# Performance work log

Measured on AMD Instinct MI355X. Metric: run time of the kernel, lower is better.

Reference implementation:

```python
import jax, jax.numpy as jnp
import numpy as np

B, T, C, H = 8, 2048, 1024, 64

def setup_inputs() -> dict:
    key = jax.random.key(0)
    k1, k2, k3, k4 = jax.random.split(key, 4)
    sc = 1.0 / np.sqrt(C)
    return {
        "x": jax.random.normal(k1, (B, T, C), dtype=jnp.float32),
        "Wk": jax.random.normal(k2, (C, H), dtype=jnp.float32) * sc,
        "Wq": jax.random.normal(k3, (C, H), dtype=jnp.float32) * sc,
        "Wv": jax.random.normal(k4, (C, H), dtype=jnp.float32) * sc,
    }

def reference(x, Wk, Wq, Wv):
    # bias-free projections: [B,T,C] @ [C,H] -> [B,T,H]
    k = jnp.einsum("btc,ch->bth", x, Wk)
    q = jnp.einsum("btc,ch->bth", x, Wq)
    v = jnp.einsum("btc,ch->bth", x, Wv)
    scale = Wk.shape[-1] ** -0.5  # head_size ** -0.5
    # attention scores [B,T,T]
    wei = jnp.einsum("bth,bsh->bts", q, k) * scale
    # causal mask: position t attends to s <= t
    Tn = x.shape[1]
    causal = jnp.tril(jnp.ones((Tn, Tn), dtype=bool))
    wei = jnp.where(causal[None, :, :], wei, jnp.float32(-jnp.inf))
    wei = jax.nn.softmax(wei, axis=-1)
    out = jnp.einsum("bts,bsh->bth", wei, v)  # [B,T,H]
    return out
```

## Files before the change

### kernel.cpp

```cpp
#include <hip/hip_runtime.h>
#include <math.h>

#define Bb 8
#define Tt 2048
#define Cc 1024
#define Hh 64

typedef __attribute__((ext_vector_type(8))) short short8;
typedef __attribute__((ext_vector_type(4))) float f32x4;

static __device__ __forceinline__ unsigned short f2bf(float f) {
    union { float f; unsigned u; } v; v.f = f;
    unsigned r = (v.u + 0x7FFFu + ((v.u >> 16) & 1u)) >> 16;
    return (unsigned short)r;
}

__global__ __launch_bounds__(256)
void wconv_kernel(const float* __restrict__ Wk, const float* __restrict__ Wq,
                  const float* __restrict__ Wv, unsigned short* __restrict__ WbT)
{
    const int n = blockIdx.x;
    const int h = n & 63;
    const float* W; float scale = 1.0f;
    if (n < 64)       { W = Wq; scale = 0.125f; }
    else if (n < 128) { W = Wk; }
    else              { W = Wv; }
    #pragma unroll
    for (int i = 0; i < 4; ++i) {
        const int k = threadIdx.x + (i << 8);
        WbT[n * 1024 + k] = f2bf(W[k * 64 + h] * scale);
    }
}

__global__ __launch_bounds__(512)
void proj_kernel(const float* __restrict__ x, const unsigned short* __restrict__ WbT,
                 unsigned short* __restrict__ qb, unsigned short* __restrict__ kb,
                 unsigned short* __restrict__ vb)
{
    __shared__ unsigned short As[64][72];
    __shared__ unsigned short Bs[192][72];

    const int tid  = threadIdx.x;
    const int row0 = blockIdx.x * 64;
    const int lane = tid & 63;
    const int w    = tid >> 6;
    const int wm   = w >> 2;
    const int wn   = w & 3;
    const int fr   = lane & 15;
    const int fko  = (lane >> 4) << 3;

    f32x4 acc[2][3];
    #pragma unroll
    for (int i = 0; i < 2; ++i)
        #pragma unroll
        for (int j = 0; j < 3; ++j) acc[i][j] = (f32x4){0.f, 0.f, 0.f, 0.f};

    for (int k0 = 0; k0 < Cc; k0 += 64) {
        #pragma unroll
        for (int i = 0; i < 2; ++i) {
            const int c  = tid + (i << 9);
            const int r  = c >> 4;
            const int ko = (c & 15) << 2;
            const float4 xv = *reinterpret_cast<const float4*>(
                &x[(size_t)(row0 + r) * Cc + k0 + ko]);
            ushort4 h4;
            h4.x = f2bf(xv.x); h4.y = f2bf(xv.y); h4.z = f2bf(xv.z); h4.w = f2bf(xv.w);
            *reinterpret_cast<ushort4*>(&As[r][ko]) = h4;
        }
        #pragma unroll
        for (int i = 0; i < 3; ++i) {
            const int c  = tid + (i << 9);
            const int r  = c >> 3;
            const int ko = (c & 7) << 3;
            const short8 bv = *reinterpret_cast<const short8*>(
                &WbT[(size_t)r * 1024 + k0 + ko]);
            *reinterpret_cast<short8*>(&Bs[r][ko]) = bv;
        }
        __syncthreads();

        #pragma unroll
        for (int sub = 0; sub < 2; ++sub) {
            short8 af[2], bf[3];
            #pragma unroll
            for (int mf = 0; mf < 2; ++mf)
                af[mf] = *reinterpret_cast<const short8*>(
                    &As[wm * 32 + mf * 16 + fr][sub * 32 + fko]);
            #pragma unroll
            for (int nf = 0; nf < 3; ++nf)
                bf[nf] = *reinterpret_cast<const short8*>(
                    &Bs[wn * 48 + nf * 16 + fr][sub * 32 + fko]);
            #pragma unroll
            for (int mf = 0; mf < 2; ++mf)
                #pragma unroll
                for (int nf = 0; nf < 3; ++nf)
                    acc[mf][nf] = __builtin_amdgcn_mfma_f32_16x16x32_bf16(
                        af[mf], bf[nf], acc[mf][nf], 0, 0, 0);
        }
        __syncthreads();
    }

    #pragma unroll
    for (int mf = 0; mf < 2; ++mf)
        #pragma unroll
        for (int nf = 0; nf < 3; ++nf) {
            const int col = wn * 48 + nf * 16 + fr;
            const int mat = col >> 6;
            const int h   = col & 63;
            unsigned short* dst = (mat == 0) ? qb : (mat == 1) ? kb : vb;
            #pragma unroll
            for (int r = 0; r < 4; ++r) {
                const int row = row0 + wm * 32 + mf * 16 + ((lane >> 4) << 2) + r;
                dst[(size_t)row * 64 + h] = f2bf(acc[mf][nf][r]);
            }
        }
}

__global__ __launch_bounds__(256)
void vtrans_kernel(const unsigned short* __restrict__ vb,
                   unsigned short* __restrict__ vt)
{
    __shared__ unsigned short ls[64][72];
    const int tid = threadIdx.x;
    const int t0  = blockIdx.x * 64;
    const int b   = blockIdx.y;

    #pragma unroll
    for (int i = 0; i < 2; ++i) {
        const int c  = tid + (i << 8);
        const int r  = c >> 3;
        const int ho = (c & 7) << 3;
        *reinterpret_cast<short8*>(&ls[r][ho]) =
            *reinterpret_cast<const short8*>(&vb[((size_t)b * Tt + t0 + r) * 64 + ho]);
    }
    __syncthreads();
    #pragma unroll
    for (int i = 0; i < 2; ++i) {
        const int c  = tid + (i << 8);
        const int h  = c >> 3;
        const int to = (c & 7) << 3;
        short8 v;
        #pragma unroll
        for (int j = 0; j < 8; ++j) v[j] = (short)ls[to + j][h];
        *reinterpret_cast<short8*>(&vt[((size_t)b * 64 + h) * Tt + t0 + to]) = v;
    }
}

__global__ __launch_bounds__(256)
void attn_kernel(const unsigned short* __restrict__ qb,
                 const unsigned short* __restrict__ kb,
                 const unsigned short* __restrict__ vt,
                 float* __restrict__ out)
{
    __shared__ float smem[9216];

    const int tid  = threadIdx.x;
    const int b    = blockIdx.y;
    const int qt   = 63 - blockIdx.x;
    const int lane = tid & 63;
    const int w    = tid >> 6;
    const int fr   = lane & 15;
    const int fg   = lane >> 4;
    const int fko  = fg << 3;
    const int ktmax = qt >> 1;

    short8 aq[2][2];
    #pragma unroll
    for (int mf = 0; mf < 2; ++mf)
        #pragma unroll
        for (int hs = 0; hs < 2; ++hs) {
            const size_t gq = (size_t)b * Tt + qt * 32 + mf * 16 + fr;
            aq[mf][hs] = *reinterpret_cast<const short8*>(&qb[gq * 64 + hs * 32 + fko]);
        }

    float mrun[2][4], lrun[2][4];
    f32x4 O[2][4];
    #pragma unroll
    for (int mf = 0; mf < 2; ++mf) {
        #pragma unroll
        for (int r = 0; r < 4; ++r) { mrun[mf][r] = -INFINITY; lrun[mf][r] = 0.f; }
        #pragma unroll
        for (int nh = 0; nh < 4; ++nh) O[mf][nh] = (f32x4){0.f, 0.f, 0.f, 0.f};
    }

    unsigned short* Pw = (unsigned short*)smem + w * 2304;

    for (int kt = w; kt <= ktmax; kt += 4) {
        short8 bk[4][2], bv[4][2];
        #pragma unroll
        for (int nf = 0; nf < 4; ++nf)
            #pragma unroll
            for (int hs = 0; hs < 2; ++hs) {
                const size_t gk = (size_t)b * Tt + kt * 64 + nf * 16 + fr;
                bk[nf][hs] = *reinterpret_cast<const short8*>(&kb[gk * 64 + hs * 32 + fko]);
            }
        #pragma unroll
        for (int nh = 0; nh < 4; ++nh)
            #pragma unroll
            for (int ks = 0; ks < 2; ++ks) {
                const size_t gv = ((size_t)b * 64 + nh * 16 + fr) * Tt
                                  + kt * 64 + ks * 32 + fko;
                bv[nh][ks] = *reinterpret_cast<const short8*>(&vt[gv]);
            }

        const f32x4 zero = (f32x4){0.f, 0.f, 0.f, 0.f};
        f32x4 s[2][4];
        #pragma unroll
        for (int mf = 0; mf < 2; ++mf)
            #pragma unroll
            for (int nf = 0; nf < 4; ++nf) {
                f32x4 t = __builtin_amdgcn_mfma_f32_16x16x32_bf16(aq[mf][0], bk[nf][0], zero, 0, 0, 0);
                s[mf][nf] = __builtin_amdgcn_mfma_f32_16x16x32_bf16(aq[mf][1], bk[nf][1], t, 0, 0, 0);
            }

        if (kt == ktmax) {
            #pragma unroll
            for (int mf = 0; mf < 2; ++mf)
                #pragma unroll
                for (int nf = 0; nf < 4; ++nf)
                    #pragma unroll
                    for (int r = 0; r < 4; ++r) {
                        const int key  = kt * 64 + nf * 16 + fr;
                        const int qrow = qt * 32 + mf * 16 + (fg << 2) + r;
                        if (key > qrow) s[mf][nf][r] = -INFINITY;
                    }
        }

        float alpha[2][4];
        #pragma unroll
        for (int mf = 0; mf < 2; ++mf)
            #pragma unroll
            for (int r = 0; r < 4; ++r) {
                float tmax = fmaxf(fmaxf(s[mf][0][r], s[mf][1][r]),
                                   fmaxf(s[mf][2][r], s[mf][3][r]));
                #pragma unroll
                for (int off = 1; off < 16; off <<= 1)
                    tmax = fmaxf(tmax, __shfl_xor(tmax, off, 64));
                const float mn = fmaxf(mrun[mf][r], tmax);
                const float al = __expf(mrun[mf][r] - mn);
                float ps = 0.f;
                #pragma unroll
                for (int nf = 0; nf < 4; ++nf) {
                    const float pv = __expf(s[mf][nf][r] - mn);
                    s[mf][nf][r] = pv;
                    ps += pv;
                }
                #pragma unroll
                for (int off = 1; off < 16; off <<= 1)
                    ps += __shfl_xor(ps, off, 64);
                lrun[mf][r] = lrun[mf][r] * al + ps;
                mrun[mf][r] = mn;
                alpha[mf][r] = al;
            }

        #pragma unroll
        for (int mf = 0; mf < 2; ++mf)
            #pragma unroll
            for (int nf = 0; nf < 4; ++nf)
                #pragma unroll
                for (int r = 0; r < 4; ++r)
                    Pw[(mf * 16 + (fg << 2) + r) * 72 + nf * 16 + fr] = f2bf(s[mf][nf][r]);

        #pragma unroll
        for (int mf = 0; mf < 2; ++mf) {
            const f32x4 av = (f32x4){alpha[mf][0], alpha[mf][1], alpha[mf][2], alpha[mf][3]};
            #pragma unroll
            for (int nh = 0; nh < 4; ++nh) O[mf][nh] *= av;
        }
        short8 pa[2][2];
        #pragma unroll
        for (int mf = 0; mf < 2; ++mf)
            #pragma unroll
            for (int ks = 0; ks < 2; ++ks)
                pa[mf][ks] = *reinterpret_cast<const short8*>(
                    &Pw[(mf * 16 + fr) * 72 + ks * 32 + fko]);
        #pragma unroll
        for (int mf = 0; mf < 2; ++mf)
            #pragma unroll
            for (int nh = 0; nh < 4; ++nh) {
                O[mf][nh] = __builtin_amdgcn_mfma_f32_16x16x32_bf16(pa[mf][0], bv[nh][0], O[mf][nh], 0, 0, 0);
                O[mf][nh] = __builtin_amdgcn_mfma_f32_16x16x32_bf16(pa[mf][1], bv[nh][1], O[mf][nh], 0, 0, 0);
            }
    }

    __syncthreads();
    float* Om = smem;
    float* Ms = smem + 8704;
    float* Ls = smem + 8832;
    #pragma unroll
    for (int mf = 0; mf < 2; ++mf)
        #pragma unroll
        for (int nh = 0; nh < 4; ++nh)
            #pragma unroll
            for (int r = 0; r < 4; ++r)
                Om[(w * 32 + mf * 16 + (fg << 2) + r) * 68 + nh * 16 + fr] = O[mf][nh][r];
    if (fr == 0) {
        #pragma unroll
        for (int mf = 0; mf < 2; ++mf)
            #pragma unroll
            for (int r = 0; r < 4; ++r) {
                Ms[w * 32 + mf * 16 + (fg << 2) + r] = mrun[mf][r];
                Ls[w * 32 + mf * 16 + (fg << 2) + r] = lrun[mf][r];
            }
    }
    __syncthreads();

    const int row = tid >> 3;
    const int h0  = (tid & 7) << 3;
    float M = -INFINITY;
    #pragma unroll
    for (int ww = 0; ww < 4; ++ww) M = fmaxf(M, Ms[ww * 32 + row]);
    float L = 0.f, o[8];
    #pragma unroll
    for (int j = 0; j < 8; ++j) o[j] = 0.f;
    #pragma unroll
    for (int ww = 0; ww < 4; ++ww) {
        const float sc = __expf(Ms[ww * 32 + row] - M);
        L += Ls[ww * 32 + row] * sc;
        const float4 a = *reinterpret_cast<const float4*>(&Om[(ww * 32 + row) * 68 + h0]);
        const float4 c = *reinterpret_cast<const float4*>(&Om[(ww * 32 + row) * 68 + h0 + 4]);
        o[0] += a.x * sc; o[1] += a.y * sc; o[2] += a.z * sc; o[3] += a.w * sc;
        o[4] += c.x * sc; o[5] += c.y * sc; o[6] += c.z * sc; o[7] += c.w * sc;
    }
    const float invL = 1.f / L;
    float* dst = &out[((size_t)b * Tt + qt * 32 + row) * 64 + h0];
    *reinterpret_cast<float4*>(dst)     = make_float4(o[0]*invL, o[1]*invL, o[2]*invL, o[3]*invL);
    *reinterpret_cast<float4*>(dst + 4) = make_float4(o[4]*invL, o[5]*invL, o[6]*invL, o[7]*invL);
}

extern "C" void kernel_launch(void* const* d_in, const int* in_sizes, int n_in,
                              void* d_out, int out_size, void* d_ws, size_t ws_size,
                              hipStream_t stream)
{
    const float* x  = (const float*)d_in[0];
    const float* Wk = (const float*)d_in[1];
    const float* Wq = (const float*)d_in[2];
    const float* Wv = (const float*)d_in[3];
    float* out = (float*)d_out;

    const size_t n = (size_t)Bb * Tt * Hh;
    unsigned short* WbT = (unsigned short*)d_ws;
    unsigned short* qb  = WbT + 196608;
    unsigned short* kb  = qb + n;
    unsigned short* vb  = kb + n;
    unsigned short* vt  = vb + n;

    wconv_kernel <<<dim3(192),      256, 0, stream>>>(Wk, Wq, Wv, WbT);
    proj_kernel  <<<dim3(256),      512, 0, stream>>>(x, WbT, qb, kb, vb);
    vtrans_kernel<<<dim3(32, 8),    256, 0, stream>>>(vb, vt);
    attn_kernel  <<<dim3(64, 8),    256, 0, stream>>>(qb, kb, vt, out);
}
```

Baseline: 154.5 us.

## Fuse V transpose into projection, transpose score layout, use exp2 softmax

The projection kernel now uses 32-row tiles with 256 threads and 512 blocks, and writes V straight into transposed layout, so the separate vtrans kernel and its round trip are gone. In the attention kernel, scores are computed as K·Q^T so each lane owns a single query row. That cuts the row max/sum reductions to two cross-lane shuffles and lets P be stored to LDS as packed 4-wide writes. The softmax scale folds log2(e) into Wq and uses exp2f, and the grid is flattened so batches interleave across consecutive blocks. In exchange, alpha now has to be redistributed to O's row layout with shuffles, and the smaller projection tiles reload the weight tile more often.

```diff
diff --git a/kernel.cpp b/kernel.cpp
--- a/kernel.cpp
+++ b/kernel.cpp
@@ -11,9 +11,10 @@
 
 static __device__ __forceinline__ unsigned short f2bf(float f) {
     union { float f; unsigned u; } v; v.f = f;
-    unsigned r = (v.u + 0x7FFFu + ((v.u >> 16) & 1u)) >> 16;
-    return (unsigned short)r;
-}
+    return (unsigned short)((v.u + 0x7FFFu + ((v.u >> 16) & 1u)) >> 16);
+}
+
+#define LOG2E 1.44269504088896340736f
 
 __global__ __launch_bounds__(256)
 void wconv_kernel(const float* __restrict__ Wk, const float* __restrict__ Wq,
@@ -22,7 +23,7 @@
     const int n = blockIdx.x;
     const int h = n & 63;
     const float* W; float scale = 1.0f;
-    if (n < 64)       { W = Wq; scale = 0.125f; }
+    if (n < 64)       { W = Wq; scale = 0.125f * LOG2E; }
     else if (n < 128) { W = Wk; }
     else              { W = Wv; }
     #pragma unroll
@@ -32,22 +33,21 @@
     }
 }
 
-__global__ __launch_bounds__(512)
+__global__ __launch_bounds__(256)
 void proj_kernel(const float* __restrict__ x, const unsigned short* __restrict__ WbT,
                  unsigned short* __restrict__ qb, unsigned short* __restrict__ kb,
-                 unsigned short* __restrict__ vb)
+                 unsigned short* __restrict__ vt)
 {
-    __shared__ unsigned short As[64][72];
+    __shared__ unsigned short As[32][72];
     __shared__ unsigned short Bs[192][72];
 
     const int tid  = threadIdx.x;
-    const int row0 = blockIdx.x * 64;
+    const int row0 = blockIdx.x * 32;
     const int lane = tid & 63;
     const int w    = tid >> 6;
-    const int wm   = w >> 2;
-    const int wn   = w & 3;
     const int fr   = lane & 15;
-    const int fko  = (lane >> 4) << 3;
+    const int fg   = lane >> 4;
+    const int fko  = fg << 3;
 
     f32x4 acc[2][3];
     #pragma unroll
@@ -56,25 +56,26 @@
         for (int j = 0; j < 3; ++j) acc[i][j] = (f32x4){0.f, 0.f, 0.f, 0.f};
 
     for (int k0 = 0; k0 < Cc; k0 += 64) {
-        #pragma unroll
-        for (int i = 0; i < 2; ++i) {
-            const int c  = tid + (i << 9);
-            const int r  = c >> 4;
-            const int ko = (c & 15) << 2;
-            const float4 xv = *reinterpret_cast<const float4*>(
-                &x[(size_t)(row0 + r) * Cc + k0 + ko]);
-            ushort4 h4;
-            h4.x = f2bf(xv.x); h4.y = f2bf(xv.y); h4.z = f2bf(xv.z); h4.w = f2bf(xv.w);
-            *reinterpret_cast<ushort4*>(&As[r][ko]) = h4;
-        }
-        #pragma unroll
-        for (int i = 0; i < 3; ++i) {
-            const int c  = tid + (i << 9);
+        {
+            const int r  = tid >> 3;
+            const int ko = (tid & 7) << 3;
+            const float* src = &x[(size_t)(row0 + r) * Cc + k0 + ko];
+            const float4 a0 = *reinterpret_cast<const float4*>(src);
+            const float4 a1 = *reinterpret_cast<const float4*>(src + 4);
+            short8 h8;
+            h8[0] = (short)f2bf(a0.x); h8[1] = (short)f2bf(a0.y);
+            h8[2] = (short)f2bf(a0.z); h8[3] = (short)f2bf(a0.w);
+            h8[4] = (short)f2bf(a1.x); h8[5] = (short)f2bf(a1.y);
+            h8[6] = (short)f2bf(a1.z); h8[7] = (short)f2bf(a1.w);
+            *reinterpret_cast<short8*>(&As[r][ko]) = h8;
+        }
+        #pragma unroll
+        for (int i = 0; i < 6; ++i) {
+            const int c  = tid + (i << 8);
             const int r  = c >> 3;
             const int ko = (c & 7) << 3;
-            const short8 bv = *reinterpret_cast<const short8*>(
-                &WbT[(size_t)r * 1024 + k0 + ko]);
-            *reinterpret_cast<short8*>(&Bs[r][ko]) = bv;
+            *reinterpret_cast<short8*>(&Bs[r][ko]) =
+                *reinterpret_cast<const short8*>(&WbT[(size_t)r * 1024 + k0 + ko]);
         }
         __syncthreads();
 
@@ -84,11 +85,11 @@
             #pragma unroll
             for (int mf = 0; mf < 2; ++mf)
                 af[mf] = *reinterpret_cast<const short8*>(
-                    &As[wm * 32 + mf * 16 + fr][sub * 32 + fko]);
+                    &As[mf * 16 + fr][sub * 32 + fko]);
             #pragma unroll
             for (int nf = 0; nf < 3; ++nf)
                 bf[nf] = *reinterpret_cast<const short8*>(
-                    &Bs[wn * 48 + nf * 16 + fr][sub * 32 + fko]);
+                    &Bs[w * 48 + nf * 16 + fr][sub * 32 + fko]);
             #pragma unroll
             for (int mf = 0; mf < 2; ++mf)
                 #pragma unroll
@@ -103,46 +104,24 @@
     for (int mf = 0; mf < 2; ++mf)
         #pragma unroll
         for (int nf = 0; nf < 3; ++nf) {
-            const int col = wn * 48 + nf * 16 + fr;
-            const int mat = col >> 6;
-            const int h   = col & 63;
-            unsigned short* dst = (mat == 0) ? qb : (mat == 1) ? kb : vb;
-            #pragma unroll
-            for (int r = 0; r < 4; ++r) {
-                const int row = row0 + wm * 32 + mf * 16 + ((lane >> 4) << 2) + r;
-                dst[(size_t)row * 64 + h] = f2bf(acc[mf][nf][r]);
-            }
-        }
-}
-
-__global__ __launch_bounds__(256)
-void vtrans_kernel(const unsigned short* __restrict__ vb,
-                   unsigned short* __restrict__ vt)
-{
-    __shared__ unsigned short ls[64][72];
-    const int tid = threadIdx.x;
-    const int t0  = blockIdx.x * 64;
-    const int b   = blockIdx.y;
-
-    #pragma unroll
-    for (int i = 0; i < 2; ++i) {
-        const int c  = tid + (i << 8);
-        const int r  = c >> 3;
-        const int ho = (c & 7) << 3;
-        *reinterpret_cast<short8*>(&ls[r][ho]) =
-            *reinterpret_cast<const short8*>(&vb[((size_t)b * Tt + t0 + r) * 64 + ho]);
-    }
-    __syncthreads();
-    #pragma unroll
-    for (int i = 0; i < 2; ++i) {
-        const int c  = tid + (i << 8);
-        const int h  = c >> 3;
-        const int to = (c & 7) << 3;
-        short8 v;
-        #pragma unroll
-        for (int j = 0; j < 8; ++j) v[j] = (short)ls[to + j][h];
-        *reinterpret_cast<short8*>(&vt[((size_t)b * 64 + h) * Tt + t0 + to]) = v;
-    }
+            const int col  = w * 48 + nf * 16 + fr;
+            const int mat  = col >> 6;
+            const int h    = col & 63;
+            const int rowb = row0 + mf * 16 + (fg << 2);
+            if (mat == 2) {
+                const int bb = rowb >> 11;
+                const int t  = rowb & 2047;
+                ushort4 pk;
+                pk.x = f2bf(acc[mf][nf][0]); pk.y = f2bf(acc[mf][nf][1]);
+                pk.z = f2bf(acc[mf][nf][2]); pk.w = f2bf(acc[mf][nf][3]);
+                *reinterpret_cast<ushort4*>(&vt[((size_t)bb * 64 + h) * Tt + t]) = pk;
+            } else {
+                unsigned short* dst = mat ? kb : qb;
+                #pragma unroll
+                for (int r = 0; r < 4; ++r)
+                    dst[(size_t)(rowb + r) * 64 + h] = f2bf(acc[mf][nf][r]);
+            }
+        }
 }
 
 __global__ __launch_bounds__(256)
@@ -154,8 +133,9 @@
     __shared__ float smem[9216];
 
     const int tid  = threadIdx.x;
-    const int b    = blockIdx.y;
-    const int qt   = 63 - blockIdx.x;
+    const int fid  = blockIdx.x;
+    const int b    = fid & 7;
+    const int qt   = 63 - (fid >> 3);
     const int lane = tid & 63;
     const int w    = tid >> 6;
     const int fr   = lane & 15;
@@ -165,33 +145,30 @@
 
     short8 aq[2][2];
     #pragma unroll
+    for (int n = 0; n < 2; ++n)
+        #pragma unroll
+        for (int hs = 0; hs < 2; ++hs) {
+            const size_t gq = (size_t)b * Tt + qt * 32 + n * 16 + fr;
+            aq[n][hs] = *reinterpret_cast<const short8*>(&qb[gq * 64 + hs * 32 + fko]);
+        }
+
+    float mrun[2] = {-INFINITY, -INFINITY}, lrun[2] = {0.f, 0.f};
+    f32x4 O[2][4];
+    #pragma unroll
     for (int mf = 0; mf < 2; ++mf)
         #pragma unroll
-        for (int hs = 0; hs < 2; ++hs) {
-            const size_t gq = (size_t)b * Tt + qt * 32 + mf * 16 + fr;
-            aq[mf][hs] = *reinterpret_cast<const short8*>(&qb[gq * 64 + hs * 32 + fko]);
-        }
-
-    float mrun[2][4], lrun[2][4];
-    f32x4 O[2][4];
-    #pragma unroll
-    for (int mf = 0; mf < 2; ++mf) {
-        #pragma unroll
-        for (int r = 0; r < 4; ++r) { mrun[mf][r] = -INFINITY; lrun[mf][r] = 0.f; }
-        #pragma unroll
         for (int nh = 0; nh < 4; ++nh) O[mf][nh] = (f32x4){0.f, 0.f, 0.f, 0.f};
-    }
 
     unsigned short* Pw = (unsigned short*)smem + w * 2304;
 
     for (int kt = w; kt <= ktmax; kt += 4) {
         short8 bk[4][2], bv[4][2];
         #pragma unroll
-        for (int nf = 0; nf < 4; ++nf)
+        for (int kf = 0; kf < 4; ++kf)
             #pragma unroll
             for (int hs = 0; hs < 2; ++hs) {
-                const size_t gk = (size_t)b * Tt + kt * 64 + nf * 16 + fr;
-                bk[nf][hs] = *reinterpret_cast<const short8*>(&kb[gk * 64 + hs * 32 + fko]);
+                const size_t gk = (size_t)b * Tt + kt * 64 + kf * 16 + fr;
+                bk[kf][hs] = *reinterpret_cast<const short8*>(&kb[gk * 64 + hs * 32 + fko]);
             }
         #pragma unroll
         for (int nh = 0; nh < 4; ++nh)
@@ -203,69 +180,77 @@
             }
 
         const f32x4 zero = (f32x4){0.f, 0.f, 0.f, 0.f};
-        f32x4 s[2][4];
-        #pragma unroll
-        for (int mf = 0; mf < 2; ++mf)
-            #pragma unroll
-            for (int nf = 0; nf < 4; ++nf) {
-                f32x4 t = __builtin_amdgcn_mfma_f32_16x16x32_bf16(aq[mf][0], bk[nf][0], zero, 0, 0, 0);
-                s[mf][nf] = __builtin_amdgcn_mfma_f32_16x16x32_bf16(aq[mf][1], bk[nf][1], t, 0, 0, 0);
+        f32x4 st[4][2];
+        #pragma unroll
+        for (int kf = 0; kf < 4; ++kf)
+            #pragma unroll
+            for (int n = 0; n < 2; ++n) {
+                f32x4 t = __builtin_amdgcn_mfma_f32_16x16x32_bf16(bk[kf][0], aq[n][0], zero, 0, 0, 0);
+                st[kf][n] = __builtin_amdgcn_mfma_f32_16x16x32_bf16(bk[kf][1], aq[n][1], t, 0, 0, 0);
             }
 
         if (kt == ktmax) {
             #pragma unroll
-            for (int mf = 0; mf < 2; ++mf)
-                #pragma unroll
-                for (int nf = 0; nf < 4; ++nf)
+            for (int kf = 0; kf < 4; ++kf)
+                #pragma unroll
+                for (int n = 0; n < 2; ++n)
                     #pragma unroll
                     for (int r = 0; r < 4; ++r) {
-                        const int key  = kt * 64 + nf * 16 + fr;
-                        const int qrow = qt * 32 + mf * 16 + (fg << 2) + r;
-                        if (key > qrow) s[mf][nf][r] = -INFINITY;
+                        const int key  = kt * 64 + kf * 16 + (fg << 2) + r;
+                        const int qrow = qt * 32 + n * 16 + fr;
+                        if (key > qrow) st[kf][n][r] = -INFINITY;
                     }
         }
 
-        float alpha[2][4];
-        #pragma unroll
-        for (int mf = 0; mf < 2; ++mf)
-            #pragma unroll
-            for (int r = 0; r < 4; ++r) {
-                float tmax = fmaxf(fmaxf(s[mf][0][r], s[mf][1][r]),
-                                   fmaxf(s[mf][2][r], s[mf][3][r]));
-                #pragma unroll
-                for (int off = 1; off < 16; off <<= 1)
-                    tmax = fmaxf(tmax, __shfl_xor(tmax, off, 64));
-                const float mn = fmaxf(mrun[mf][r], tmax);
-                const float al = __expf(mrun[mf][r] - mn);
-                float ps = 0.f;
-                #pragma unroll
-                for (int nf = 0; nf < 4; ++nf) {
-                    const float pv = __expf(s[mf][nf][r] - mn);
-                    s[mf][nf][r] = pv;
-                    ps += pv;
+        float alpha[2];
+        #pragma unroll
+        for (int n = 0; n < 2; ++n) {
+            float tmax = -INFINITY;
+            #pragma unroll
+            for (int kf = 0; kf < 4; ++kf)
+                #pragma unroll
+                for (int r = 0; r < 4; ++r) tmax = fmaxf(tmax, st[kf][n][r]);
+            tmax = fmaxf(tmax, __shfl_xor(tmax, 16, 64));
+            tmax = fmaxf(tmax, __shfl_xor(tmax, 32, 64));
+            const float mn = fmaxf(mrun[n], tmax);
+            const float al = exp2f(mrun[n] - mn);
+            float psum = 0.f;
+            #pragma unroll
+            for (int kf = 0; kf < 4; ++kf)
+                #pragma unroll
+                for (int r = 0; r < 4; ++r) {
+                    const float pv = exp2f(st[kf][n][r] - mn);
+                    st[kf][n][r] = pv;
+                    psum += pv;
                 }
-                #pragma unroll
-                for (int off = 1; off < 16; off <<= 1)
-                    ps += __shfl_xor(ps, off, 64);
-                lrun[mf][r] = lrun[mf][r] * al + ps;
-                mrun[mf][r] = mn;
-                alpha[mf][r] = al;
-            }
-
-        #pragma unroll
-        for (int mf = 0; mf < 2; ++mf)
-            #pragma unroll
-            for (int nf = 0; nf < 4; ++nf)
-                #pragma unroll
-                for (int r = 0; r < 4; ++r)
-                    Pw[(mf * 16 + (fg << 2) + r) * 72 + nf * 16 + fr] = f2bf(s[mf][nf][r]);
+            psum += __shfl_xor(psum, 16, 64);
+            psum += __shfl_xor(psum, 32, 64);
+            lrun[n] = lrun[n] * al + psum;
+            mrun[n] = mn;
+            alpha[n] = al;
+        }
+
+        #pragma unroll
+        for (int kf = 0; kf < 4; ++kf)
+            #pragma unroll
+            for (int n = 0; n < 2; ++n) {
+                ushort4 pk;
+                pk.x = f2bf(st[kf][n][0]); pk.y = f2bf(st[kf][n][1]);
+                pk.z = f2bf(st[kf][n][2]); pk.w = f2bf(st[kf][n][3]);
+                *reinterpret_cast<ushort4*>(
+                    &Pw[(n * 16 + fr) * 72 + kf * 16 + (fg << 2)]) = pk;
+            }
 
         #pragma unroll
         for (int mf = 0; mf < 2; ++mf) {
-            const f32x4 av = (f32x4){alpha[mf][0], alpha[mf][1], alpha[mf][2], alpha[mf][3]};
+            f32x4 av;
+            #pragma unroll
+            for (int r = 0; r < 4; ++r)
+                av[r] = __shfl(alpha[mf], (fg << 2) + r, 64);
             #pragma unroll
             for (int nh = 0; nh < 4; ++nh) O[mf][nh] *= av;
         }
+
         short8 pa[2][2];
         #pragma unroll
         for (int mf = 0; mf < 2; ++mf)
@@ -293,14 +278,12 @@
             #pragma unroll
             for (int r = 0; r < 4; ++r)
                 Om[(w * 32 + mf * 16 + (fg << 2) + r) * 68 + nh * 16 + fr] = O[mf][nh][r];
-    if (fr == 0) {
-        #pragma unroll
-        for (int mf = 0; mf < 2; ++mf)
-            #pragma unroll
-            for (int r = 0; r < 4; ++r) {
-                Ms[w * 32 + mf * 16 + (fg << 2) + r] = mrun[mf][r];
-                Ls[w * 32 + mf * 16 + (fg << 2) + r] = lrun[mf][r];
-            }
+    if (fg == 0) {
+        #pragma unroll
+        for (int n = 0; n < 2; ++n) {
+            Ms[w * 32 + n * 16 + fr] = mrun[n];
+            Ls[w * 32 + n * 16 + fr] = lrun[n];
+        }
     }
     __syncthreads();
 
@@ -314,7 +297,7 @@
     for (int j = 0; j < 8; ++j) o[j] = 0.f;
     #pragma unroll
     for (int ww = 0; ww < 4; ++ww) {
-        const float sc = __expf(Ms[ww * 32 + row] - M);
+        const float sc = exp2f(Ms[ww * 32 + row] - M);
         L += Ls[ww * 32 + row] * sc;
         const float4 a = *reinterpret_cast<const float4*>(&Om[(ww * 32 + row) * 68 + h0]);
         const float4 c = *reinterpret_cast<const float4*>(&Om[(ww * 32 + row) * 68 + h0 + 4]);
@@ -341,11 +324,9 @@
     unsigned short* WbT = (unsigned short*)d_ws;
     unsigned short* qb  = WbT + 196608;
     unsigned short* kb  = qb + n;
-    unsigned short* vb  = kb + n;
-    unsigned short* vt  = vb + n;
-
-    wconv_kernel <<<dim3(192),      256, 0, stream>>>(Wk, Wq, Wv, WbT);
-    proj_kernel  <<<dim3(256),      512, 0, stream>>>(x, WbT, qb, kb, vb);
-    vtrans_kernel<<<dim3(32, 8),    256, 0, stream>>>(vb, vt);
-    attn_kernel  <<<dim3(64, 8),    256, 0, stream>>>(qb, kb, vt, out);
-}
+    unsigned short* vt  = kb + n;
+
+    wconv_kernel<<<dim3(192), 256, 0, stream>>>(Wk, Wq, Wv, WbT);
+    proj_kernel <<<dim3(512), 256, 0, stream>>>(x, WbT, qb, kb, vt);
+    attn_kernel <<<dim3(512), 256, 0, stream>>>(qb, kb, vt, out);
+}
```

Result: faster. 140.5 us (-9.0%).
